# Performance work log

Measured on AMD Instinct MI355X. Metric: run time of the kernel, lower is better.

The kernel has to match this reference:

```python
import jax, jax.numpy as jnp
import numpy as np

B, SX, SY, D, H = 4, 4096, 4096, 1024, 64


def setup_inputs() -> dict:
    key = jax.random.key(0)
    ks = jax.random.split(key, 7)
    x = jax.random.normal(ks[0], (B, SX, D), dtype=jnp.float32)
    y = jax.random.normal(ks[1], (B, SY, D), dtype=jnp.float32)
    valid_lens_x = jax.random.randint(ks[2], (B,), 1, SX + 1).astype(jnp.int64)
    valid_lens_y = jax.random.randint(ks[3], (B,), 1, SY + 1).astype(jnp.int64)
    s = 1.0 / np.sqrt(D)
    Wq = jax.random.uniform(ks[4], (D, H), jnp.float32, -s, s)
    Wk = jax.random.uniform(ks[5], (D, H), jnp.float32, -s, s)
    Wv = jax.random.uniform(ks[6], (D, H), jnp.float32, -s, s)
    return {"x": x, "y": y, "valid_lens_x": valid_lens_x,
            "valid_lens_y": valid_lens_y, "use_causal": 1,
            "Wq": Wq, "Wk": Wk, "Wv": Wv}


def reference(x, y, valid_lens_x, valid_lens_y, use_causal, Wq, Wk, Wv):
    # projections (Linear, no bias)
    k = x @ Wk                      # [B, Sx, H]
    q = y @ Wq                      # [B, Sy, H]
    v = x @ Wv                      # [B, Sx, H]
    scale = k.shape[-1] ** -0.5
    wei = jnp.einsum('bqh,bkh->bqk', q, k) * scale   # [B, Sy, Sx]
    Sq, Sk = q.shape[1], k.shape[1]
    if use_causal:  # static python int -> tril masked_fill branch
        tril = jnp.tril(jnp.ones((Sq, Sk), dtype=bool))
        wei = jnp.where(tril[None], wei, -jnp.inf)
    # per-sample valid-length cross mask
    kmask = jnp.arange(Sk)[None, :] < valid_lens_x[:, None]   # [B, Sk]
    qmask = jnp.arange(Sq)[None, :] < valid_lens_y[:, None]   # [B, Sq]
    mask = qmask[:, :, None] & kmask[:, None, :]              # [B, Sq, Sk]
    wei = jnp.where(mask, wei, -jnp.inf)
    # NaN-safe softmax: zero out fully-masked rows
    row_mask = jnp.all(jnp.isinf(wei), axis=2, keepdims=True)  # [B, Sq, 1]
    safe = jnp.where(row_mask, 0.0, wei)
    probs = jax.nn.softmax(safe, axis=2)
    probs = jnp.where(row_mask, 0.0, probs)
    # dropout p=0.0 -> identity (eval)
    out = probs @ v                 # [B, Sy, H]
    return out
```

## Files before the change

### kernel.cpp

```cpp
#include <hip/hip_runtime.h>
#include <hip/hip_bf16.h>
#include <stdint.h>

#define BB 4
#define SXN 4096
#define SYN 4096
#define DD 1024
#define HH 64

typedef float f32x4 __attribute__((ext_vector_type(4)));
typedef short bf16x8 __attribute__((ext_vector_type(8)));

static __device__ __forceinline__ unsigned short f2bf(float f) {
  unsigned int u = __float_as_uint(f);
  u += 0x7fffu + ((u >> 16) & 1u);
  return (unsigned short)(u >> 16);
}
static __device__ __forceinline__ float bf2f(unsigned short b) {
  return __uint_as_float(((unsigned int)b) << 16);
}

__global__ __launch_bounds__(256) void prep_wt(
    const float* __restrict__ Wq, const float* __restrict__ Wk,
    const float* __restrict__ Wv, unsigned short* __restrict__ Wt) {
  int gid = blockIdx.x * 256 + threadIdx.x;
  int mat = gid >> 16;
  int h = (gid >> 10) & 63;
  int k = gid & 1023;
  const float* W = (mat == 0) ? Wk : (mat == 1) ? Wv : Wq;
  Wt[gid] = f2bf(W[k * HH + h]);
}

__global__ __launch_bounds__(256) void proj_kernel(
    const float* __restrict__ xin, const float* __restrict__ yin,
    const unsigned short* __restrict__ Wt,
    unsigned short* __restrict__ Qb, unsigned short* __restrict__ Kb,
    unsigned short* __restrict__ Vt) {
  __shared__ __align__(16) unsigned short xa[64][72];
  const int tid = threadIdx.x;
  const int w = tid >> 6;
  const int l = tid & 63;
  const int li = l & 15, lg = l >> 4;
  const int row0 = blockIdx.x * 64;
  const bool qpath = (blockIdx.y == 1);
  const float* src = qpath ? yin : xin;

  const unsigned short* WtA = qpath ? (Wt + 2 * 65536) : Wt;
  const unsigned short* WtB = Wt + 65536;

  f32x4 acc0[4], acc1[4];
  const f32x4 z4 = {0.f, 0.f, 0.f, 0.f};
#pragma unroll
  for (int i = 0; i < 4; ++i) { acc0[i] = z4; acc1[i] = z4; }

  for (int ks = 0; ks < 16; ++ks) {
#pragma unroll
    for (int p = 0; p < 4; ++p) {
      int r = p * 16 + (tid >> 4);
      int c = (tid & 15) * 4;
      const float4 v = *reinterpret_cast<const float4*>(
          &src[(size_t)(row0 + r) * DD + ks * 64 + c]);
      ushort4 o;
      o.x = f2bf(v.x); o.y = f2bf(v.y); o.z = f2bf(v.z); o.w = f2bf(v.w);
      *reinterpret_cast<ushort4*>(&xa[r][c]) = o;
    }
    __syncthreads();

    const bf16x8 a0 = *reinterpret_cast<const bf16x8*>(&xa[w * 16 + li][lg * 8]);
    const bf16x8 a1 = *reinterpret_cast<const bf16x8*>(&xa[w * 16 + li][32 + lg * 8]);

#pragma unroll
    for (int hb = 0; hb < 4; ++hb) {
      const int wrow = hb * 16 + li;
      const bf16x8 b0 = *reinterpret_cast<const bf16x8*>(
          &WtA[wrow * 1024 + ks * 64 + lg * 8]);
      const bf16x8 b1 = *reinterpret_cast<const bf16x8*>(
          &WtA[wrow * 1024 + ks * 64 + 32 + lg * 8]);
      acc0[hb] = __builtin_amdgcn_mfma_f32_16x16x32_bf16(a0, b0, acc0[hb], 0, 0, 0);
      acc0[hb] = __builtin_amdgcn_mfma_f32_16x16x32_bf16(a1, b1, acc0[hb], 0, 0, 0);
    }
    if (!qpath) {
#pragma unroll
      for (int hb = 0; hb < 4; ++hb) {
        const int wrow = hb * 16 + li;
        const bf16x8 b0 = *reinterpret_cast<const bf16x8*>(
            &WtB[wrow * 1024 + ks * 64 + lg * 8]);
        const bf16x8 b1 = *reinterpret_cast<const bf16x8*>(
            &WtB[wrow * 1024 + ks * 64 + 32 + lg * 8]);
        acc1[hb] = __builtin_amdgcn_mfma_f32_16x16x32_bf16(a0, b0, acc1[hb], 0, 0, 0);
        acc1[hb] = __builtin_amdgcn_mfma_f32_16x16x32_bf16(a1, b1, acc1[hb], 0, 0, 0);
      }
    }
    __syncthreads();
  }

  const int rbase = row0 + w * 16 + lg * 4;
  if (qpath) {
#pragma unroll
    for (int hb = 0; hb < 4; ++hb)
#pragma unroll
      for (int r = 0; r < 4; ++r)
        Qb[(size_t)(rbase + r) * HH + hb * 16 + li] = f2bf(acc0[hb][r] * 0.125f);
  } else {
#pragma unroll
    for (int hb = 0; hb < 4; ++hb)
#pragma unroll
      for (int r = 0; r < 4; ++r)
        Kb[(size_t)(rbase + r) * HH + hb * 16 + li] = f2bf(acc0[hb][r]);
    const int b = rbase >> 12;
    const int sx = rbase & 4095;
#pragma unroll
    for (int hb = 0; hb < 4; ++hb) {
      ushort4 o;
      o.x = f2bf(acc1[hb][0]); o.y = f2bf(acc1[hb][1]);
      o.z = f2bf(acc1[hb][2]); o.w = f2bf(acc1[hb][3]);
      *reinterpret_cast<ushort4*>(
          &Vt[((size_t)b * HH + hb * 16 + li) * SXN + sx]) = o;
    }
  }
}

__global__ __launch_bounds__(256) void flash_kernel(
    const unsigned short* __restrict__ Qb, const unsigned short* __restrict__ Kb,
    const unsigned short* __restrict__ Vt, const int* __restrict__ vlx_p,
    const int* __restrict__ vly_p, const int* __restrict__ uc_p,
    float* __restrict__ out) {
  __shared__ __align__(16) unsigned short Kt[64][72];
  __shared__ __align__(16) unsigned short Vl[64][72];
  __shared__ __align__(16) unsigned short Pl[4][16][72];

  const int tid = threadIdx.x;
  const int w = tid >> 6, l = tid & 63;
  const int li = l & 15, lg = l >> 4;
  const int qt = blockIdx.x, b = blockIdx.y;
  const int q0 = qt * 64;
  const int vlx = vlx_p[b], vly = vly_p[b];
  const int causal = uc_p[0];
  const float LOG2E = 1.4426950408889634f;

  float* outB = out + (size_t)b * SYN * HH;

  if (q0 >= vly) {
    const float4 z = make_float4(0.f, 0.f, 0.f, 0.f);
#pragma unroll
    for (int i = 0; i < 4; ++i)
      *reinterpret_cast<float4*>(&outB[(size_t)q0 * HH + tid * 16 + i * 4]) = z;
    return;
  }

  int kend = causal ? min(vlx, q0 + 64) : vlx;
  if (kend > SXN) kend = SXN;
  const int nsteps = (kend + 63) >> 6;

  const unsigned short* Qrow = Qb + ((size_t)b * SYN + q0 + w * 16 + li) * HH;
  const bf16x8 qa0 = *reinterpret_cast<const bf16x8*>(&Qrow[lg * 8]);
  const bf16x8 qa1 = *reinterpret_cast<const bf16x8*>(&Qrow[32 + lg * 8]);

  const unsigned short* KbB = Kb + (size_t)b * SXN * HH;
  const unsigned short* VtB = Vt + (size_t)b * HH * SXN;

  f32x4 o[4];
  float mrun[4], lrun[4];
  const f32x4 z4 = {0.f, 0.f, 0.f, 0.f};
#pragma unroll
  for (int i = 0; i < 4; ++i) { o[i] = z4; mrun[i] = -INFINITY; lrun[i] = 0.f; }

  const int qg0 = q0 + w * 16 + lg * 4;

  for (int s = 0; s < nsteps; ++s) {
    const int key0 = s << 6;
    {
      const int r = tid >> 3, c = (tid & 7) * 8;
      *reinterpret_cast<uint4*>(&Kt[r][c]) =
          *reinterpret_cast<const uint4*>(&KbB[(size_t)(key0 + r) * HH + c]);
      *reinterpret_cast<uint4*>(&Kt[r + 32][c]) =
          *reinterpret_cast<const uint4*>(&KbB[(size_t)(key0 + r + 32) * HH + c]);
      *reinterpret_cast<uint4*>(&Vl[r][c]) =
          *reinterpret_cast<const uint4*>(&VtB[(size_t)r * SXN + key0 + c]);
      *reinterpret_cast<uint4*>(&Vl[r + 32][c]) =
          *reinterpret_cast<const uint4*>(&VtB[(size_t)(r + 32) * SXN + key0 + c]);
    }
    __syncthreads();

    f32x4 sa[4];
#pragma unroll
    for (int kb = 0; kb < 4; ++kb) {
      const bf16x8 k0 = *reinterpret_cast<const bf16x8*>(&Kt[kb * 16 + li][lg * 8]);
      const bf16x8 k1 = *reinterpret_cast<const bf16x8*>(&Kt[kb * 16 + li][32 + lg * 8]);
      f32x4 acc = z4;
      acc = __builtin_amdgcn_mfma_f32_16x16x32_bf16(qa0, k0, acc, 0, 0, 0);
      acc = __builtin_amdgcn_mfma_f32_16x16x32_bf16(qa1, k1, acc, 0, 0, 0);
      sa[kb] = acc;
    }

#pragma unroll
    for (int r = 0; r < 4; ++r) {
      const int qcap = causal ? (qg0 + r) : 0x7fffffff;
      float sv[4];
#pragma unroll
      for (int kb = 0; kb < 4; ++kb) {
        const int kg = key0 + kb * 16 + li;
        const bool valid = (kg < vlx) && (kg <= qcap);
        sv[kb] = valid ? sa[kb][r] : -1e30f;
      }
      float tm = fmaxf(fmaxf(sv[0], sv[1]), fmaxf(sv[2], sv[3]));
      tm = fmaxf(tm, __shfl_xor(tm, 1));
      tm = fmaxf(tm, __shfl_xor(tm, 2));
      tm = fmaxf(tm, __shfl_xor(tm, 4));
      tm = fmaxf(tm, __shfl_xor(tm, 8));
      const float mn = fmaxf(mrun[r], tm);
      const float corr = exp2f((mrun[r] - mn) * LOG2E);
      mrun[r] = mn;
      float ps = 0.f;
#pragma unroll
      for (int kb = 0; kb < 4; ++kb) {
        const float p = exp2f((sv[kb] - mn) * LOG2E);
        const unsigned short pb = f2bf(p);
        Pl[w][lg * 4 + r][kb * 16 + li] = pb;
        ps += bf2f(pb);
      }
      ps += __shfl_xor(ps, 1);
      ps += __shfl_xor(ps, 2);
      ps += __shfl_xor(ps, 4);
      ps += __shfl_xor(ps, 8);
      lrun[r] = lrun[r] * corr + ps;
#pragma unroll
      for (int df = 0; df < 4; ++df) o[df][r] *= corr;
    }

#pragma unroll
    for (int kh = 0; kh < 2; ++kh) {
      const bf16x8 pa = *reinterpret_cast<const bf16x8*>(&Pl[w][li][kh * 32 + lg * 8]);
#pragma unroll
      for (int df = 0; df < 4; ++df) {
        const bf16x8 vb =
            *reinterpret_cast<const bf16x8*>(&Vl[df * 16 + li][kh * 32 + lg * 8]);
        o[df] = __builtin_amdgcn_mfma_f32_16x16x32_bf16(pa, vb, o[df], 0, 0, 0);
      }
    }
    __syncthreads();
  }

#pragma unroll
  for (int r = 0; r < 4; ++r) {
    const int qg = qg0 + r;
    const float inv = (lrun[r] > 0.f) ? 1.0f / lrun[r] : 0.f;
    const bool rowvalid = (qg < vly);
    float* orow = &outB[(size_t)qg * HH];
#pragma unroll
    for (int df = 0; df < 4; ++df) {
      const float val = rowvalid ? o[df][r] * inv : 0.f;
      orow[df * 16 + li] = val;
    }
  }
}

extern "C" void kernel_launch(void* const* d_in, const int* in_sizes, int n_in,
                              void* d_out, int out_size, void* d_ws, size_t ws_size,
                              hipStream_t stream) {
  const float* x = (const float*)d_in[0];
  const float* y = (const float*)d_in[1];
  const int* vlx = (const int*)d_in[2];
  const int* vly = (const int*)d_in[3];
  const int* uc = (const int*)d_in[4];
  const float* Wq = (const float*)d_in[5];
  const float* Wk = (const float*)d_in[6];
  const float* Wv = (const float*)d_in[7];
  float* out = (float*)d_out;

  char* ws = (char*)d_ws;
  unsigned short* Qb = (unsigned short*)(ws);
  unsigned short* Kb = (unsigned short*)(ws + (2u << 20));
  unsigned short* Vt = (unsigned short*)(ws + (4u << 20));
  unsigned short* Wt = (unsigned short*)(ws + (6u << 20));

  prep_wt<<<768, 256, 0, stream>>>(Wq, Wk, Wv, Wt);
  proj_kernel<<<dim3(256, 2), 256, 0, stream>>>(x, y, Wt, Qb, Kb, Vt);
  flash_kernel<<<dim3(64, 4), 256, 0, stream>>>(Qb, Kb, Vt, vlx, vly, uc, out);
}
```

Baseline: 285.4 us.

## Split flash attention KV range across waves and double-buffer projection loads

The projection kernel now stages fp32 input tiles straight into LDS with global_load_lds, using a swizzled layout and double buffering, and converts to bf16 when reading the MFMA operands. The flash kernel switches to 512-thread blocks over 32-row query tiles. Each pair of waves splits the key range into four chunks (split-K) and reads K and V directly from global memory instead of through shared memory. Partial max, sum and output are merged in LDS, and blocks are ordered heaviest-causal-first to improve load balance and occupancy. The cost is an extra reduction step, uncached global operand reads, and higher LDS use per block.

```diff
diff --git a/kernel.cpp b/kernel.cpp
--- a/kernel.cpp
+++ b/kernel.cpp
@@ -2,7 +2,7 @@
 #include <hip/hip_bf16.h>
 #include <stdint.h>
 
-#define BB 4
+#define BBATCH 4
 #define SXN 4096
 #define SYN 4096
 #define DD 1024
@@ -18,6 +18,21 @@
 }
 static __device__ __forceinline__ float bf2f(unsigned short b) {
   return __uint_as_float(((unsigned int)b) << 16);
+}
+
+static __device__ __forceinline__ bf16x8 cvt8(f32x4 lo, f32x4 hi) {
+  bf16x8 v;
+  v[0] = (short)f2bf(lo[0]); v[1] = (short)f2bf(lo[1]);
+  v[2] = (short)f2bf(lo[2]); v[3] = (short)f2bf(lo[3]);
+  v[4] = (short)f2bf(hi[0]); v[5] = (short)f2bf(hi[1]);
+  v[6] = (short)f2bf(hi[2]); v[7] = (short)f2bf(hi[3]);
+  return v;
+}
+
+static __device__ __forceinline__ void gload_lds16(const void* g, void* l) {
+  __builtin_amdgcn_global_load_lds(
+      (const __attribute__((address_space(1))) unsigned int*)g,
+      (__attribute__((address_space(3))) unsigned int*)l, 16, 0, 0);
 }
 
 __global__ __launch_bounds__(256) void prep_wt(
@@ -25,26 +40,24 @@
     const float* __restrict__ Wv, unsigned short* __restrict__ Wt) {
   int gid = blockIdx.x * 256 + threadIdx.x;
   int mat = gid >> 16;
+  int k = gid & 1023;
   int h = (gid >> 10) & 63;
-  int k = gid & 1023;
   const float* W = (mat == 0) ? Wk : (mat == 1) ? Wv : Wq;
   Wt[gid] = f2bf(W[k * HH + h]);
 }
 
-__global__ __launch_bounds__(256) void proj_kernel(
+__global__ __launch_bounds__(256, 3) void proj_kernel(
     const float* __restrict__ xin, const float* __restrict__ yin,
     const unsigned short* __restrict__ Wt,
     unsigned short* __restrict__ Qb, unsigned short* __restrict__ Kb,
     unsigned short* __restrict__ Vt) {
-  __shared__ __align__(16) unsigned short xa[64][72];
+  __shared__ __align__(16) float xa[2][64 * 64];
   const int tid = threadIdx.x;
-  const int w = tid >> 6;
-  const int l = tid & 63;
+  const int w = tid >> 6, l = tid & 63;
   const int li = l & 15, lg = l >> 4;
-  const int row0 = blockIdx.x * 64;
-  const bool qpath = (blockIdx.y == 1);
+  const bool qpath = blockIdx.x >= 256;
+  const int row0 = (qpath ? (blockIdx.x - 256) : (int)blockIdx.x) * 64;
   const float* src = qpath ? yin : xin;
-
   const unsigned short* WtA = qpath ? (Wt + 2 * 65536) : Wt;
   const unsigned short* WtB = Wt + 65536;
 
@@ -53,45 +66,48 @@
 #pragma unroll
   for (int i = 0; i < 4; ++i) { acc0[i] = z4; acc1[i] = z4; }
 
-  for (int ks = 0; ks < 16; ++ks) {
-#pragma unroll
-    for (int p = 0; p < 4; ++p) {
-      int r = p * 16 + (tid >> 4);
-      int c = (tid & 15) * 4;
-      const float4 v = *reinterpret_cast<const float4*>(
-          &src[(size_t)(row0 + r) * DD + ks * 64 + c]);
-      ushort4 o;
-      o.x = f2bf(v.x); o.y = f2bf(v.y); o.z = f2bf(v.z); o.w = f2bf(v.w);
-      *reinterpret_cast<ushort4*>(&xa[r][c]) = o;
+  auto stage = [&](int bsel, int kc) {
+#pragma unroll
+    for (int i = 0; i < 4; ++i) {
+      const int r = i * 16 + w * 4 + (l >> 4);
+      const int c16 = (l & 15) ^ (r & 7);
+      const float* g = src + (size_t)(row0 + r) * DD + kc * 64 + c16 * 4;
+      float* lp = &xa[bsel][i * 1024 + w * 256];
+      gload_lds16(g, lp);
+    }
+  };
+
+  int buf = 0;
+  stage(0, 0);
+  __syncthreads();
+  for (int kc = 0; kc < 16; ++kc) {
+    if (kc < 15) stage(buf ^ 1, kc + 1);
+    const int rrow = w * 16 + li;
+    const int swz = (rrow & 7) * 4;
+#pragma unroll
+    for (int ks = 0; ks < 2; ++ks) {
+      const int base = rrow * 64 + ks * 32 + lg * 8;
+      const f32x4 lo = *reinterpret_cast<const f32x4*>(&xa[buf][base ^ swz]);
+      const f32x4 hi = *reinterpret_cast<const f32x4*>(&xa[buf][(base + 4) ^ swz]);
+      const bf16x8 a = cvt8(lo, hi);
+      const int gks = kc * 2 + ks;
+#pragma unroll
+      for (int hb = 0; hb < 4; ++hb) {
+        const bf16x8 b0 = *reinterpret_cast<const bf16x8*>(
+            &WtA[(hb * 16 + li) * 1024 + gks * 32 + lg * 8]);
+        acc0[hb] = __builtin_amdgcn_mfma_f32_16x16x32_bf16(a, b0, acc0[hb], 0, 0, 0);
+      }
+      if (!qpath) {
+#pragma unroll
+        for (int hb = 0; hb < 4; ++hb) {
+          const bf16x8 b1 = *reinterpret_cast<const bf16x8*>(
+              &WtB[(hb * 16 + li) * 1024 + gks * 32 + lg * 8]);
+          acc1[hb] = __builtin_amdgcn_mfma_f32_16x16x32_bf16(a, b1, acc1[hb], 0, 0, 0);
+        }
+      }
     }
     __syncthreads();
-
-    const bf16x8 a0 = *reinterpret_cast<const bf16x8*>(&xa[w * 16 + li][lg * 8]);
-    const bf16x8 a1 = *reinterpret_cast<const bf16x8*>(&xa[w * 16 + li][32 + lg * 8]);
-
-#pragma unroll
-    for (int hb = 0; hb < 4; ++hb) {
-      const int wrow = hb * 16 + li;
-      const bf16x8 b0 = *reinterpret_cast<const bf16x8*>(
-          &WtA[wrow * 1024 + ks * 64 + lg * 8]);
-      const bf16x8 b1 = *reinterpret_cast<const bf16x8*>(
-          &WtA[wrow * 1024 + ks * 64 + 32 + lg * 8]);
-      acc0[hb] = __builtin_amdgcn_mfma_f32_16x16x32_bf16(a0, b0, acc0[hb], 0, 0, 0);
-      acc0[hb] = __builtin_amdgcn_mfma_f32_16x16x32_bf16(a1, b1, acc0[hb], 0, 0, 0);
-    }
-    if (!qpath) {
-#pragma unroll
-      for (int hb = 0; hb < 4; ++hb) {
-        const int wrow = hb * 16 + li;
-        const bf16x8 b0 = *reinterpret_cast<const bf16x8*>(
-            &WtB[wrow * 1024 + ks * 64 + lg * 8]);
-        const bf16x8 b1 = *reinterpret_cast<const bf16x8*>(
-            &WtB[wrow * 1024 + ks * 64 + 32 + lg * 8]);
-        acc1[hb] = __builtin_amdgcn_mfma_f32_16x16x32_bf16(a0, b0, acc1[hb], 0, 0, 0);
-        acc1[hb] = __builtin_amdgcn_mfma_f32_16x16x32_bf16(a1, b1, acc1[hb], 0, 0, 0);
-      }
-    }
-    __syncthreads();
+    buf ^= 1;
   }
 
   const int rbase = row0 + w * 16 + lg * 4;
@@ -120,41 +136,34 @@
   }
 }
 
-__global__ __launch_bounds__(256) void flash_kernel(
+__global__ __launch_bounds__(512, 4) void flash_kernel(
     const unsigned short* __restrict__ Qb, const unsigned short* __restrict__ Kb,
     const unsigned short* __restrict__ Vt, const int* __restrict__ vlx_p,
     const int* __restrict__ vly_p, const int* __restrict__ uc_p,
     float* __restrict__ out) {
-  __shared__ __align__(16) unsigned short Kt[64][72];
-  __shared__ __align__(16) unsigned short Vl[64][72];
-  __shared__ __align__(16) unsigned short Pl[4][16][72];
+  __shared__ __align__(16) unsigned short Pl[8][16][72];
+  __shared__ __align__(16) float Ol[8][16][64];
+  __shared__ float Ml[8][16], Ll[8][16];
 
   const int tid = threadIdx.x;
   const int w = tid >> 6, l = tid & 63;
   const int li = l & 15, lg = l >> 4;
-  const int qt = blockIdx.x, b = blockIdx.y;
-  const int q0 = qt * 64;
+  const int rg = w & 1, c = w >> 1;
+
+  const int kblk = blockIdx.x;
+  const int b = (kblk & 7) >> 1;
+  const int rb = 127 - (((kblk >> 3) << 1) | (kblk & 1));
+  const int q0 = rb * 32;
   const int vlx = vlx_p[b], vly = vly_p[b];
   const int causal = uc_p[0];
   const float LOG2E = 1.4426950408889634f;
 
-  float* outB = out + (size_t)b * SYN * HH;
-
-  if (q0 >= vly) {
-    const float4 z = make_float4(0.f, 0.f, 0.f, 0.f);
-#pragma unroll
-    for (int i = 0; i < 4; ++i)
-      *reinterpret_cast<float4*>(&outB[(size_t)q0 * HH + tid * 16 + i * 4]) = z;
-    return;
-  }
-
-  int kend = causal ? min(vlx, q0 + 64) : vlx;
+  const int qbase = q0 + rg * 16;
+  int kend = causal ? min(vlx, qbase + 16) : vlx;
   if (kend > SXN) kend = SXN;
-  const int nsteps = (kend + 63) >> 6;
-
-  const unsigned short* Qrow = Qb + ((size_t)b * SYN + q0 + w * 16 + li) * HH;
-  const bf16x8 qa0 = *reinterpret_cast<const bf16x8*>(&Qrow[lg * 8]);
-  const bf16x8 qa1 = *reinterpret_cast<const bf16x8*>(&Qrow[32 + lg * 8]);
+  const int nst = (kend + 63) >> 6;
+  const int s0 = (c * nst) >> 2;
+  const int s1 = ((c + 1) * nst) >> 2;
 
   const unsigned short* KbB = Kb + (size_t)b * SXN * HH;
   const unsigned short* VtB = Vt + (size_t)b * HH * SXN;
@@ -165,92 +174,120 @@
 #pragma unroll
   for (int i = 0; i < 4; ++i) { o[i] = z4; mrun[i] = -INFINITY; lrun[i] = 0.f; }
 
-  const int qg0 = q0 + w * 16 + lg * 4;
-
-  for (int s = 0; s < nsteps; ++s) {
-    const int key0 = s << 6;
-    {
-      const int r = tid >> 3, c = (tid & 7) * 8;
-      *reinterpret_cast<uint4*>(&Kt[r][c]) =
-          *reinterpret_cast<const uint4*>(&KbB[(size_t)(key0 + r) * HH + c]);
-      *reinterpret_cast<uint4*>(&Kt[r + 32][c]) =
-          *reinterpret_cast<const uint4*>(&KbB[(size_t)(key0 + r + 32) * HH + c]);
-      *reinterpret_cast<uint4*>(&Vl[r][c]) =
-          *reinterpret_cast<const uint4*>(&VtB[(size_t)r * SXN + key0 + c]);
-      *reinterpret_cast<uint4*>(&Vl[r + 32][c]) =
-          *reinterpret_cast<const uint4*>(&VtB[(size_t)(r + 32) * SXN + key0 + c]);
-    }
-    __syncthreads();
-
-    f32x4 sa[4];
-#pragma unroll
-    for (int kb = 0; kb < 4; ++kb) {
-      const bf16x8 k0 = *reinterpret_cast<const bf16x8*>(&Kt[kb * 16 + li][lg * 8]);
-      const bf16x8 k1 = *reinterpret_cast<const bf16x8*>(&Kt[kb * 16 + li][32 + lg * 8]);
-      f32x4 acc = z4;
-      acc = __builtin_amdgcn_mfma_f32_16x16x32_bf16(qa0, k0, acc, 0, 0, 0);
-      acc = __builtin_amdgcn_mfma_f32_16x16x32_bf16(qa1, k1, acc, 0, 0, 0);
-      sa[kb] = acc;
-    }
-
-#pragma unroll
-    for (int r = 0; r < 4; ++r) {
-      const int qcap = causal ? (qg0 + r) : 0x7fffffff;
-      float sv[4];
+  const bool active = (qbase < vly);
+  const int qg0 = qbase + lg * 4;
+
+  if (active && s1 > s0) {
+    const unsigned short* Qrow = Qb + ((size_t)b * SYN + qbase + li) * HH;
+    const bf16x8 qa0 = *reinterpret_cast<const bf16x8*>(&Qrow[lg * 8]);
+    const bf16x8 qa1 = *reinterpret_cast<const bf16x8*>(&Qrow[32 + lg * 8]);
+
+    for (int s = s0; s < s1; ++s) {
+      const int key0 = s << 6;
+      f32x4 sa[4];
 #pragma unroll
       for (int kb = 0; kb < 4; ++kb) {
-        const int kg = key0 + kb * 16 + li;
-        const bool valid = (kg < vlx) && (kg <= qcap);
-        sv[kb] = valid ? sa[kb][r] : -1e30f;
-      }
-      float tm = fmaxf(fmaxf(sv[0], sv[1]), fmaxf(sv[2], sv[3]));
-      tm = fmaxf(tm, __shfl_xor(tm, 1));
-      tm = fmaxf(tm, __shfl_xor(tm, 2));
-      tm = fmaxf(tm, __shfl_xor(tm, 4));
-      tm = fmaxf(tm, __shfl_xor(tm, 8));
-      const float mn = fmaxf(mrun[r], tm);
-      const float corr = exp2f((mrun[r] - mn) * LOG2E);
-      mrun[r] = mn;
-      float ps = 0.f;
-#pragma unroll
-      for (int kb = 0; kb < 4; ++kb) {
-        const float p = exp2f((sv[kb] - mn) * LOG2E);
-        const unsigned short pb = f2bf(p);
-        Pl[w][lg * 4 + r][kb * 16 + li] = pb;
-        ps += bf2f(pb);
-      }
-      ps += __shfl_xor(ps, 1);
-      ps += __shfl_xor(ps, 2);
-      ps += __shfl_xor(ps, 4);
-      ps += __shfl_xor(ps, 8);
-      lrun[r] = lrun[r] * corr + ps;
-#pragma unroll
-      for (int df = 0; df < 4; ++df) o[df][r] *= corr;
-    }
-
-#pragma unroll
-    for (int kh = 0; kh < 2; ++kh) {
-      const bf16x8 pa = *reinterpret_cast<const bf16x8*>(&Pl[w][li][kh * 32 + lg * 8]);
-#pragma unroll
-      for (int df = 0; df < 4; ++df) {
-        const bf16x8 vb =
-            *reinterpret_cast<const bf16x8*>(&Vl[df * 16 + li][kh * 32 + lg * 8]);
-        o[df] = __builtin_amdgcn_mfma_f32_16x16x32_bf16(pa, vb, o[df], 0, 0, 0);
-      }
-    }
-    __syncthreads();
-  }
-
-#pragma unroll
-  for (int r = 0; r < 4; ++r) {
-    const int qg = qg0 + r;
-    const float inv = (lrun[r] > 0.f) ? 1.0f / lrun[r] : 0.f;
-    const bool rowvalid = (qg < vly);
-    float* orow = &outB[(size_t)qg * HH];
-#pragma unroll
-    for (int df = 0; df < 4; ++df) {
-      const float val = rowvalid ? o[df][r] * inv : 0.f;
-      orow[df * 16 + li] = val;
+        const unsigned short* Kr = &KbB[(size_t)(key0 + kb * 16 + li) * HH];
+        const bf16x8 k0 = *reinterpret_cast<const bf16x8*>(&Kr[lg * 8]);
+        const bf16x8 k1 = *reinterpret_cast<const bf16x8*>(&Kr[32 + lg * 8]);
+        f32x4 acc = z4;
+        acc = __builtin_amdgcn_mfma_f32_16x16x32_bf16(qa0, k0, acc, 0, 0, 0);
+        acc = __builtin_amdgcn_mfma_f32_16x16x32_bf16(qa1, k1, acc, 0, 0, 0);
+        sa[kb] = acc;
+      }
+
+#pragma unroll
+      for (int r = 0; r < 4; ++r) {
+        const int qcap = causal ? (qg0 + r) : 0x7fffffff;
+        float sv[4];
+#pragma unroll
+        for (int kb = 0; kb < 4; ++kb) {
+          const int kg = key0 + kb * 16 + li;
+          const bool valid = (kg < vlx) && (kg <= qcap);
+          sv[kb] = valid ? sa[kb][r] : -1e30f;
+        }
+        float tm = fmaxf(fmaxf(sv[0], sv[1]), fmaxf(sv[2], sv[3]));
+        tm = fmaxf(tm, __shfl_xor(tm, 1));
+        tm = fmaxf(tm, __shfl_xor(tm, 2));
+        tm = fmaxf(tm, __shfl_xor(tm, 4));
+        tm = fmaxf(tm, __shfl_xor(tm, 8));
+        const float mn = fmaxf(mrun[r], tm);
+        const float corr = exp2f((mrun[r] - mn) * LOG2E);
+        mrun[r] = mn;
+        float ps = 0.f;
+#pragma unroll
+        for (int kb = 0; kb < 4; ++kb) {
+          const float p = exp2f((sv[kb] - mn) * LOG2E);
+          const unsigned short pb = f2bf(p);
+          Pl[w][lg * 4 + r][kb * 16 + li] = pb;
+          ps += bf2f(pb);
+        }
+        ps += __shfl_xor(ps, 1);
+        ps += __shfl_xor(ps, 2);
+        ps += __shfl_xor(ps, 4);
+        ps += __shfl_xor(ps, 8);
+        lrun[r] = lrun[r] * corr + ps;
+#pragma unroll
+        for (int df = 0; df < 4; ++df) o[df][r] *= corr;
+      }
+
+#pragma unroll
+      for (int kh = 0; kh < 2; ++kh) {
+        const bf16x8 pa =
+            *reinterpret_cast<const bf16x8*>(&Pl[w][li][kh * 32 + lg * 8]);
+#pragma unroll
+        for (int df = 0; df < 4; ++df) {
+          const bf16x8 vb = *reinterpret_cast<const bf16x8*>(
+              &VtB[(size_t)(df * 16 + li) * SXN + key0 + kh * 32 + lg * 8]);
+          o[df] = __builtin_amdgcn_mfma_f32_16x16x32_bf16(pa, vb, o[df], 0, 0, 0);
+        }
+      }
+    }
+  }
+
+  if (active) {
+#pragma unroll
+    for (int df = 0; df < 4; ++df)
+#pragma unroll
+      for (int r = 0; r < 4; ++r)
+        Ol[w][lg * 4 + r][df * 16 + li] = o[df][r];
+    if (li == 0) {
+#pragma unroll
+      for (int r = 0; r < 4; ++r) {
+        Ml[w][lg * 4 + r] = mrun[r];
+        Ll[w][lg * 4 + r] = lrun[r];
+      }
+    }
+  }
+  __syncthreads();
+
+  {
+    float* outB = out + (size_t)b * SYN * HH;
+#pragma unroll
+    for (int i = 0; i < 4; ++i) {
+      const int rr = w * 4 + i;
+      const int mrg = rr >> 4;
+      const int rowIdx = rr & 15;
+      const int q = q0 + rr;
+      float res = 0.f;
+      if (q < vly) {
+        float M = -INFINITY;
+#pragma unroll
+        for (int cc = 0; cc < 4; ++cc)
+          M = fmaxf(M, Ml[(cc << 1) | mrg][rowIdx]);
+        if (M > -1e37f) {
+          float lsum = 0.f, acc = 0.f;
+#pragma unroll
+          for (int cc = 0; cc < 4; ++cc) {
+            const int ww = (cc << 1) | mrg;
+            const float wt = exp2f((Ml[ww][rowIdx] - M) * LOG2E);
+            lsum += wt * Ll[ww][rowIdx];
+            acc += wt * Ol[ww][rowIdx][l];
+          }
+          res = (lsum > 0.f) ? acc / lsum : 0.f;
+        }
+      }
+      outB[(size_t)q * HH + l] = res;
     }
   }
 }
@@ -275,6 +312,6 @@
   unsigned short* Wt = (unsigned short*)(ws + (6u << 20));
 
   prep_wt<<<768, 256, 0, stream>>>(Wq, Wk, Wv, Wt);
-  proj_kernel<<<dim3(256, 2), 256, 0, stream>>>(x, y, Wt, Qb, Kb, Vt);
-  flash_kernel<<<dim3(64, 4), 256, 0, stream>>>(Qb, Kb, Vt, vlx, vly, uc, out);
-}
+  proj_kernel<<<512, 256, 0, stream>>>(x, y, Wt, Qb, Kb, Vt);
+  flash_kernel<<<512, 512, 0, stream>>>(Qb, Kb, Vt, vlx, vly, uc, out);
+}
```

Measured after the change: 268.0 us. 1.07x faster.
